# Optimization experiments

Measured on AMD Instinct MI355X. Metric: run time of the kernel, lower is better.

## Reference

```python
import jax, jax.numpy as jnp
import numpy as np

N, T, DF, H, NH, E = 512, 60, 6, 64, 2, 8192
NEG = -1e10

def _leaky(x):
    return jnp.where(x >= 0, x, 0.01 * x)

def _ln(x, g, b, eps=1e-5):
    m = x.mean(-1, keepdims=True)
    v = ((x - m) ** 2).mean(-1, keepdims=True)
    return (x - m) / jnp.sqrt(v + eps) * g + b

def _gru_layer(xs, wih, whh, bih, bhh):
    # xs: (N, T, H_in) -> (N, T, H); torch GRU gate math
    h0 = jnp.zeros((xs.shape[0], whh.shape[1]), xs.dtype)
    def step(h, xt):
        gi = xt @ wih.T + bih
        gh = h @ whh.T + bhh
        ir, iz, inn = jnp.split(gi, 3, -1)
        hr, hz, hn = jnp.split(gh, 3, -1)
        r = jax.nn.sigmoid(ir + hr)
        z = jax.nn.sigmoid(iz + hz)
        n = jnp.tanh(inn + r * hn)
        h = (1 - z) * n + z * h
        return h, h
    _, hs = jax.lax.scan(step, h0, jnp.swapaxes(xs, 0, 1))
    return jnp.swapaxes(hs, 0, 1)

def _forward(x, edge_index, fc_in_w, fc_in_b, gru_wih0, gru_whh0, gru_bih0, gru_bhh0, gru_wih1, gru_whh1, gru_bih1, gru_bhh1, dm_qw, dm_kw, dm_vw, dm_vb, ssa_qw, ssa_kw, ssa_vw, ssa_vb, ln1_g, ln1_b, ln2_g, ln2_b, mlp_w1, mlp_b1, mlp_w2, mlp_b2, mha_in_w, mha_in_b, mha_out_w, mha_out_b, gf_xs_w, gf_xt_w, gf_xt_b, gf_h_w, gf_h_b, lin_w, lin_b):
    h = x @ fc_in_w.T + fc_in_b                      # (N, T, H)
    # temporal encoder: 2-layer GRU + leaky relu
    g = _gru_layer(h, gru_wih0, gru_whh0, gru_bih0, gru_bhh0)
    g = _gru_layer(g, gru_wih1, gru_whh1, gru_bih1, gru_bhh1)
    ts = _leaky(g)
    res_ts = ts[:, -1, :]                            # (N, H)
    # spatial sparse transformer: time T acts as batch, attention over stocks N
    xs = jnp.swapaxes(h, 0, 1)                       # (T, N, H)
    hd = H // NH
    q = (xs @ dm_qw.T).reshape(T, N, NH, hd).transpose(0, 2, 1, 3)
    k = (xs @ dm_kw.T).reshape(T, N, NH, hd).transpose(0, 2, 1, 3)
    v = (xs @ dm_vw.T + dm_vb).reshape(T, N, NH, hd).transpose(0, 2, 1, 3)
    attn = jnp.einsum('thnd,thmd->thnm', q, k) * (H ** -0.5)  # scale uses full dim C, as in source
    dmask = attn >= attn.mean(-1, keepdims=True)     # dynamic per-row mean threshold
    attn_s = jax.nn.softmax(jnp.where(dmask, attn, NEG), axis=-1)
    dyn = jnp.einsum('thnm,thmd->thnd', attn_s, v).transpose(0, 2, 1, 3).reshape(T, N, H)
    # SSA: static graph mask from edge_index
    qs = xs @ ssa_qw.T
    ks2 = xs @ ssa_kw.T
    vs = xs @ ssa_vw.T + ssa_vb
    a2 = jnp.einsum('tnc,tmc->tnm', qs, ks2) * (H ** -0.5)
    adj = jnp.zeros((N, N), jnp.float32).at[edge_index[0], edge_index[1]].add(1.0)
    gmask = adj >= 1.0
    a2s = jax.nn.softmax(jnp.where(gmask[None, :, :], a2, NEG), axis=-1)
    stat = jnp.einsum('tnm,tmc->tnc', a2s, vs)
    residual = dyn + stat + xs
    o = _ln(residual, ln1_g, ln1_b)
    o = (o @ mlp_w1.T + mlp_b1) @ mlp_w2.T + mlp_b2  # two linears, no activation (as in source)
    o = _ln(o + residual, ln2_g, ln2_b)
    move = _leaky(o)                                 # (T, N, H)
    # spatial embedding aggregation: sinusoidal PE + 1-head MHA over time
    pos = jnp.arange(T, dtype=jnp.float32)[:, None]
    div = jnp.exp(jnp.arange(0, H, 2, dtype=jnp.float32) * (-np.log(10000.0) / H))
    pe = jnp.zeros((T, H), jnp.float32).at[:, 0::2].set(jnp.sin(pos * div)).at[:, 1::2].set(jnp.cos(pos * div))
    src = move + pe[:, None, :]
    mq, mk, mv = jnp.split(src @ mha_in_w.T + mha_in_b, 3, axis=-1)
    sc = jnp.einsum('tnh,snh->nts', mq, mk) * (H ** -0.5)
    mo = jnp.einsum('nts,snh->tnh', jax.nn.softmax(sc, -1), mv) @ mha_out_w.T + mha_out_b
    agg = mo[-1]                                     # (N, H)
    mu = agg.mean(-1, keepdims=True)
    var = ((agg - mu) ** 2).mean(-1, keepdims=True)
    agg = (agg - mu) / jnp.sqrt(var + 1e-5)          # param-free layer_norm
    # gated fusion
    zg = jax.nn.sigmoid(agg @ gf_xs_w.T + res_ts @ gf_xt_w.T + gf_xt_b)
    fused = _leaky((zg * agg + (1 - zg) * res_ts) @ gf_h_w.T + gf_h_b)
    out = (fused @ lin_w.T + lin_b)[:, 0]
    return out, attn_s

def setup_inputs() -> dict:
    key = jax.random.key(0)
    ks = jax.random.split(key, 40)
    def w(i, shape):
        return jax.random.normal(ks[i], shape, jnp.float32) * 0.05
    return {
        'x': jax.random.normal(ks[0], (N, T, DF), jnp.float32),
        'edge_index': jax.random.randint(ks[1], (2, E), 0, N),
        'fc_in_w': w(2, (H, DF)), 'fc_in_b': w(3, (H,)),
        'gru_wih0': w(4, (3 * H, H)), 'gru_whh0': w(5, (3 * H, H)), 'gru_bih0': w(6, (3 * H,)), 'gru_bhh0': w(7, (3 * H,)),
        'gru_wih1': w(8, (3 * H, H)), 'gru_whh1': w(9, (3 * H, H)), 'gru_bih1': w(10, (3 * H,)), 'gru_bhh1': w(11, (3 * H,)),
        'dm_qw': w(12, (H, H)), 'dm_kw': w(13, (H, H)), 'dm_vw': w(14, (H, H)), 'dm_vb': w(15, (H,)),
        'ssa_qw': w(16, (H, H)), 'ssa_kw': w(17, (H, H)), 'ssa_vw': w(18, (H, H)), 'ssa_vb': w(19, (H,)),
        'ln1_g': jnp.ones((H,), jnp.float32), 'ln1_b': jnp.zeros((H,), jnp.float32),
        'ln2_g': jnp.ones((H,), jnp.float32), 'ln2_b': jnp.zeros((H,), jnp.float32),
        'mlp_w1': w(20, (2 * H, H)), 'mlp_b1': w(21, (2 * H,)), 'mlp_w2': w(22, (H, 2 * H)), 'mlp_b2': w(23, (H,)),
        'mha_in_w': w(24, (3 * H, H)), 'mha_in_b': w(25, (3 * H,)), 'mha_out_w': w(26, (H, H)), 'mha_out_b': w(27, (H,)),
        'gf_xs_w': w(28, (H, H)), 'gf_xt_w': w(29, (H, H)), 'gf_xt_b': w(30, (H,)),
        'gf_h_w': w(31, (H, H)), 'gf_h_b': w(32, (H,)),
        'lin_w': w(33, (1, H)), 'lin_b': w(34, (1,)),
    }

def reference(x, edge_index, fc_in_w, fc_in_b, gru_wih0, gru_whh0, gru_bih0, gru_bhh0, gru_wih1, gru_whh1, gru_bih1, gru_bhh1, dm_qw, dm_kw, dm_vw, dm_vb, ssa_qw, ssa_kw, ssa_vw, ssa_vb, ln1_g, ln1_b, ln2_g, ln2_b, mlp_w1, mlp_b1, mlp_w2, mlp_b2, mha_in_w, mha_in_b, mha_out_w, mha_out_b, gf_xs_w, gf_xt_w, gf_xt_b, gf_h_w, gf_h_b, lin_w, lin_b):
    return _forward(x, edge_index, fc_in_w, fc_in_b, gru_wih0, gru_whh0, gru_bih0, gru_bhh0, gru_wih1, gru_whh1, gru_bih1, gru_bhh1, dm_qw, dm_kw, dm_vw, dm_vb, ssa_qw, ssa_kw, ssa_vw, ssa_vb, ln1_g, ln1_b, ln2_g, ln2_b, mlp_w1, mlp_b1, mlp_w2, mlp_b2, mha_in_w, mha_in_b, mha_out_w, mha_out_b, gf_xs_w, gf_xt_w, gf_xt_b, gf_h_w, gf_h_b, lin_w, lin_b)
```

## Files before the change

kernel.cpp:

```cpp
#include <hip/hip_runtime.h>
#include <hip/hip_bf16.h>

#define NN 512
#define TT 60
#define DFF 6
#define EE 8192
#define TN (TT*NN)
#define TCH 20
#define NCHK 3
#define SCALEV 0.125f
#define NEGV -1.0e10f

typedef __hip_bfloat16 bf16;
using bfrag8 = __attribute__((ext_vector_type(8))) short;
using facc4  = __attribute__((ext_vector_type(4))) float;

__device__ __forceinline__ float b2f(bf16 v){ return __bfloat162float(v); }
__device__ __forceinline__ bf16 f2b(float v){ return __float2bfloat16(v); }
__device__ __forceinline__ float lk(float x){ return x >= 0.f ? x : 0.01f*x; }
__device__ __forceinline__ float sgm(float x){ return 1.f/(1.f+__expf(-x)); }

__device__ __forceinline__ float ldf(const float* p, long i){ return p[i]; }
__device__ __forceinline__ float ldf(const bf16* p, long i){ return b2f(p[i]); }
__device__ __forceinline__ void stf(float* p, long i, float v){ p[i] = v; }
__device__ __forceinline__ void stf(bf16* p, long i, float v){ p[i] = f2b(v); }

__device__ __forceinline__ float4 ld4f(const float* p){ return *(const float4*)p; }
__device__ __forceinline__ float4 ld4f(const bf16* p){
  ushort4 u = *(const ushort4*)p;
  float4 f;
  f.x = b2f(*(const bf16*)&u.x);
  f.y = b2f(*(const bf16*)&u.y);
  f.z = b2f(*(const bf16*)&u.z);
  f.w = b2f(*(const bf16*)&u.w);
  return f;
}

__device__ __forceinline__ float wsum64(float v){
  #pragma unroll
  for (int off = 32; off; off >>= 1) v += __shfl_xor(v, off, 64);
  return v;
}
__device__ __forceinline__ float wmax64(float v){
  #pragma unroll
  for (int off = 32; off; off >>= 1) v = fmaxf(v, __shfl_xor(v, off, 64));
  return v;
}

__global__ __launch_bounds__(256) void k_pack(
  const float* __restrict__ qw, const float* __restrict__ kw,
  const float* __restrict__ qsw, const float* __restrict__ ksw,
  const float* __restrict__ vw, const float* __restrict__ vsw,
  const float* __restrict__ vb, const float* __restrict__ vsb,
  const int* __restrict__ ei, unsigned int* __restrict__ msk,
  float* __restrict__ Wall, float* __restrict__ bcV)
{
  __shared__ unsigned int lmsk[8192];
  int tid = threadIdx.x;
  if (blockIdx.x == 97) {
    for (int i = tid; i < 8192; i += 256) lmsk[i] = 0u;
    __syncthreads();
    for (int e = tid; e < EE; e += 256) {
      int u = ei[e], v = ei[EE + e];
      atomicOr(&lmsk[u*16 + (v >> 5)], 1u << (v & 31));
    }
    __syncthreads();
    for (int i = tid; i < 8192; i += 256) msk[i] = lmsk[i];
    return;
  }
  int idx = blockIdx.x*256 + tid;
  if (idx < 6*4096) {
    int which = idx >> 12, rem = idx & 4095;
    const float* s = (which==0)?qw:(which==1)?kw:(which==2)?qsw:(which==3)?ksw:(which==4)?vw:vsw;
    Wall[idx] = s[rem];
  } else if (idx < 6*4096 + 128) {
    int o = idx - 6*4096;
    bcV[o] = (o < 64) ? vb[o] : vsb[o-64];
  }
}

__global__ __launch_bounds__(256) void k_fcin(
  const float* __restrict__ x, const float* __restrict__ w, const float* __restrict__ b,
  float* __restrict__ xs, float* __restrict__ resid)
{
  long idx = (long)blockIdx.x*256 + threadIdx.x;
  int o = idx & 63;
  long r = idx >> 6;
  int t = (int)(r / NN), n = (int)(r % NN);
  const float* xr = x + ((long)n*TT + t)*DFF;
  const float* wr = w + o*DFF;
  float acc = 0.f;
  #pragma unroll
  for (int j = 0; j < DFF; ++j) acc = fmaf(xr[j], wr[j], acc);
  float h = __fadd_rn(acc, b[o]);
  xs[idx] = h;
  resid[idx] = h;
}

__global__ __launch_bounds__(256) void k_proj(
  const float* __restrict__ A, const float* __restrict__ Wall, const float* __restrict__ bcV,
  float* __restrict__ qkx, float* __restrict__ qkc, bf16* __restrict__ vvc)
{
  __shared__ float As[64][68];
  __shared__ float Bs[64][68];
  int rt = blockIdx.x, bcn = blockIdx.y;
  const float* B = Wall + bcn*4096;
  int tid = threadIdx.x;
  int tx = tid & 15, ty = tid >> 4;
  float acc[4][4] = {{0.f}};
  #pragma unroll
  for (int i = 0; i < 4; ++i) {
    int t = i*256 + tid;
    int m = t >> 4, kq = (t & 15)*4;
    float4 av = *(const float4*)&A[(long)(rt*64 + m)*64 + kq];
    As[kq+0][m] = av.x; As[kq+1][m] = av.y; As[kq+2][m] = av.z; As[kq+3][m] = av.w;
    float4 bv = *(const float4*)&B[(long)m*64 + kq];
    Bs[kq+0][m] = bv.x; Bs[kq+1][m] = bv.y; Bs[kq+2][m] = bv.z; Bs[kq+3][m] = bv.w;
  }
  __syncthreads();
  for (int kk = 0; kk < 64; ++kk) {
    float4 a4 = *(const float4*)&As[kk][ty*4];
    float4 b4 = *(const float4*)&Bs[kk][tx*4];
    acc[0][0] = fmaf(a4.x,b4.x,acc[0][0]); acc[0][1] = fmaf(a4.x,b4.y,acc[0][1]); acc[0][2] = fmaf(a4.x,b4.z,acc[0][2]); acc[0][3] = fmaf(a4.x,b4.w,acc[0][3]);
    acc[1][0] = fmaf(a4.y,b4.x,acc[1][0]); acc[1][1] = fmaf(a4.y,b4.y,acc[1][1]); acc[1][2] = fmaf(a4.y,b4.z,acc[1][2]); acc[1][3] = fmaf(a4.y,b4.w,acc[1][3]);
    acc[2][0] = fmaf(a4.z,b4.x,acc[2][0]); acc[2][1] = fmaf(a4.z,b4.y,acc[2][1]); acc[2][2] = fmaf(a4.z,b4.z,acc[2][2]); acc[2][3] = fmaf(a4.z,b4.w,acc[2][3]);
    acc[3][0] = fmaf(a4.w,b4.x,acc[3][0]); acc[3][1] = fmaf(a4.w,b4.y,acc[3][1]); acc[3][2] = fmaf(a4.w,b4.z,acc[3][2]); acc[3][3] = fmaf(a4.w,b4.w,acc[3][3]);
  }
  if (bcn < 4) {
    float* C = (bcn < 2) ? qkx : qkc;
    int cb = (bcn & 1)*64;
    #pragma unroll
    for (int i = 0; i < 4; ++i) {
      long ro = (long)(rt*64 + ty*4 + i)*128 + cb + tx*4;
      #pragma unroll
      for (int j = 0; j < 4; ++j) C[ro + j] = acc[i][j];
    }
  } else {
    int cb = (bcn - 4)*64;
    float bv[4];
    #pragma unroll
    for (int j = 0; j < 4; ++j) bv[j] = bcV[cb + tx*4 + j];
    #pragma unroll
    for (int i = 0; i < 4; ++i) {
      long ro = (long)(rt*64 + ty*4 + i)*128 + cb + tx*4;
      #pragma unroll
      for (int j = 0; j < 4; ++j) vvc[ro + j] = f2b(acc[i][j] + bv[j]);
    }
  }
}

template<typename TA, typename TC>
__global__ __launch_bounds__(256) void k_gemm(
  const TA* __restrict__ A, const float* __restrict__ B, const float* __restrict__ bias,
  TC* __restrict__ C, int KD, int NC, int gather)
{
  __shared__ float As[64][68];
  __shared__ float Bs[64][68];
  int rt = blockIdx.x, bcn = blockIdx.y;
  int tid = threadIdx.x;
  int tx = tid & 15, ty = tid >> 4;
  float acc[4][4] = {{0.f}};
  int nch = KD >> 6;
  for (int kc = 0; kc < nch; ++kc) {
    __syncthreads();
    #pragma unroll
    for (int i = 0; i < 4; ++i) {
      int t = i*256 + tid;
      int m = t >> 4, kq = (t & 15)*4;
      long aoff;
      int r = rt*64 + m;
      if (gather) { int n2 = r / TT, t2 = r - n2*TT; aoff = ((long)t2*NN + n2)*64 + kc*64 + kq; }
      else aoff = (long)r*KD + kc*64 + kq;
      float4 av = ld4f(A + aoff);
      As[kq+0][m] = av.x; As[kq+1][m] = av.y; As[kq+2][m] = av.z; As[kq+3][m] = av.w;
      int col = bcn*64 + m;
      float4 bv = *(const float4*)&B[(long)col*KD + kc*64 + kq];
      Bs[kq+0][m] = bv.x; Bs[kq+1][m] = bv.y; Bs[kq+2][m] = bv.z; Bs[kq+3][m] = bv.w;
    }
    __syncthreads();
    #pragma unroll 8
    for (int kk = 0; kk < 64; ++kk) {
      float4 a4 = *(const float4*)&As[kk][ty*4];
      float4 b4 = *(const float4*)&Bs[kk][tx*4];
      acc[0][0] += a4.x*b4.x; acc[0][1] += a4.x*b4.y; acc[0][2] += a4.x*b4.z; acc[0][3] += a4.x*b4.w;
      acc[1][0] += a4.y*b4.x; acc[1][1] += a4.y*b4.y; acc[1][2] += a4.y*b4.z; acc[1][3] += a4.y*b4.w;
      acc[2][0] += a4.z*b4.x; acc[2][1] += a4.z*b4.y; acc[2][2] += a4.z*b4.z; acc[2][3] += a4.z*b4.w;
      acc[3][0] += a4.w*b4.x; acc[3][1] += a4.w*b4.y; acc[3][2] += a4.w*b4.z; acc[3][3] += a4.w*b4.w;
    }
  }
  float bv[4];
  #pragma unroll
  for (int j = 0; j < 4; ++j) bv[j] = bias ? bias[bcn*64 + tx*4 + j] : 0.f;
  #pragma unroll
  for (int i = 0; i < 4; ++i) {
    long ro = (long)(rt*64 + ty*4 + i)*NC + bcn*64 + tx*4;
    #pragma unroll
    for (int j = 0; j < 4; ++j) stf(C, ro + j, acc[i][j] + bv[j]);
  }
}

__global__ __launch_bounds__(192) void k_gru(
  const float* __restrict__ gi, const float* __restrict__ whh, const float* __restrict__ bhh,
  bf16* __restrict__ g_out, float* __restrict__ res_out, int layer)
{
  int n = blockIdx.x;
  int tid = threadIdx.x;
  int g = tid >> 6, o = tid & 63;
  __shared__ __align__(16) float h_lds[64];
  __shared__ float ghs[3][64];
  float4 w4[16];
  #pragma unroll
  for (int k4 = 0; k4 < 16; ++k4)
    w4[k4] = *(const float4*)&whh[(long)(g*64+o)*64 + k4*4];
  float bh = bhh[g*64+o];
  float ir = 0.f, iz = 0.f, inn = 0.f;
  if (tid < 64) {
    h_lds[tid] = 0.f;
    const float* gp = gi + ((long)n*TT + 0)*192;
    ir = gp[o]; iz = gp[64+o]; inn = gp[128+o];
  }
  __syncthreads();
  const float4* h4 = (const float4*)h_lds;
  for (int t = 0; t < TT; ++t) {
    float p0 = 0.f, p1 = 0.f, p2 = 0.f, p3 = 0.f;
    #pragma unroll
    for (int k4 = 0; k4 < 16; ++k4) {
      float4 hv = h4[k4];
      p0 = fmaf(w4[k4].x, hv.x, p0);
      p1 = fmaf(w4[k4].y, hv.y, p1);
      p2 = fmaf(w4[k4].z, hv.z, p2);
      p3 = fmaf(w4[k4].w, hv.w, p3);
    }
    ghs[g][o] = bh + ((p0 + p1) + (p2 + p3));
    __syncthreads();
    if (tid < 64) {
      float r = sgm(ir + ghs[0][o]);
      float z = sgm(iz + ghs[1][o]);
      float nn2 = tanhf(inn + r*ghs[2][o]);
      float hn = (1.f - z)*nn2 + z*h_lds[o];
      h_lds[o] = hn;
      if (layer == 0) g_out[((long)t*NN + n)*64 + o] = f2b(hn);
      else if (t == TT-1) res_out[(long)n*64 + o] = lk(hn);
      if (t + 1 < TT) {
        const float* gp = gi + ((long)n*TT + t + 1)*192;
        ir = gp[o]; iz = gp[64+o]; inn = gp[128+o];
      }
    }
    __syncthreads();
  }
}

#define MULADD4(QV, KV) \
  v0 = __fadd_rn(v0, __fmul_rn((QV).x, (KV).x)); \
  v1 = __fadd_rn(v1, __fmul_rn((QV).y, (KV).y)); \
  v2 = __fadd_rn(v2, __fmul_rn((QV).z, (KV).z)); \
  v3 = __fadd_rn(v3, __fmul_rn((QV).w, (KV).w));

__global__ __launch_bounds__(256, 3) void k_attn(
  const float* __restrict__ qkx, const float* __restrict__ qkc,
  const bf16* __restrict__ vvc, const unsigned int* __restrict__ msk,
  float* __restrict__ attn_out, float* __restrict__ resid,
  float* __restrict__ resid2, int tc)
{
  __shared__ __align__(16) char smem[52288];
  int bid = blockIdx.x;
  int vid = (bid & 7)*240 + (bid >> 3);
  int lt = vid / 96;
  int rem = vid - lt*96;
  int yy = rem >> 5;
  int qt = rem & 31;
  int gt = tc*TCH + lt;
  int tid = threadIdx.x, tx = tid & 31, grp = tid >> 5;
  int qbase = grp*2;

  if (yy == 2) {
    float* kc  = (float*)smem;
    bf16*  vTh = (bf16*)smem;
    float* qtl = (float*)(smem + 34816);
    bf16*  P   = (bf16*)(smem + 34816);

    float4* q4 = (float4*)qtl;
    float4* k4 = (float4*)kc;

    {
      int m = tid >> 4, jc = tid & 15;
      q4[m*17 + jc] = *(const float4*)(qkc + ((long)(lt*NN + qt*16 + m))*128 + jc*4);
    }

    float S[2][16];
    for (int p = 0; p < 4; ++p) {
      __syncthreads();
      for (int i = tid; i < 2048; i += 256) {
        int m = i >> 4, jc = i & 15;
        k4[m*17 + (jc ^ ((m >> 2) & 3))] =
          *(const float4*)(qkc + ((long)(lt*NN + p*128 + m))*128 + 64 + jc*4);
      }
      __syncthreads();
      float acc00 = 0.f, acc01 = 0.f, acc02 = 0.f, acc03 = 0.f;
      float acc10 = 0.f, acc11 = 0.f, acc12 = 0.f, acc13 = 0.f;
      #pragma unroll 4
      for (int jc = 0; jc < 16; ++jc) {
        float4 q0 = q4[(qbase+0)*17 + jc];
        float4 q1 = q4[(qbase+1)*17 + jc];
        float4 kv;
        int m0 = tx;
        kv = k4[m0*17 + (jc ^ ((m0 >> 2) & 3))];
        acc00 += q0.x*kv.x + q0.y*kv.y + q0.z*kv.z + q0.w*kv.w;
        acc10 += q1.x*kv.x + q1.y*kv.y + q1.z*kv.z + q1.w*kv.w;
        int m1 = tx + 32;
        kv = k4[m1*17 + (jc ^ ((m1 >> 2) & 3))];
        acc01 += q0.x*kv.x + q0.y*kv.y + q0.z*kv.z + q0.w*kv.w;
        acc11 += q1.x*kv.x + q1.y*kv.y + q1.z*kv.z + q1.w*kv.w;
        int m2 = tx + 64;
        kv = k4[m2*17 + (jc ^ ((m2 >> 2) & 3))];
        acc02 += q0.x*kv.x + q0.y*kv.y + q0.z*kv.z + q0.w*kv.w;
        acc12 += q1.x*kv.x + q1.y*kv.y + q1.z*kv.z + q1.w*kv.w;
        int m3 = tx + 96;
        kv = k4[m3*17 + (jc ^ ((m3 >> 2) & 3))];
        acc03 += q0.x*kv.x + q0.y*kv.y + q0.z*kv.z + q0.w*kv.w;
        acc13 += q1.x*kv.x + q1.y*kv.y + q1.z*kv.z + q1.w*kv.w;
      }
      S[0][p*4+0] = acc00; S[0][p*4+1] = acc01; S[0][p*4+2] = acc02; S[0][p*4+3] = acc03;
      S[1][p*4+0] = acc10; S[1][p*4+1] = acc11; S[1][p*4+2] = acc12; S[1][p*4+3] = acc13;
    }
    __syncthreads();

    #pragma unroll
    for (int qi = 0; qi < 2; ++qi) {
      #pragma unroll
      for (int ig = 0; ig < 16; ++ig) S[qi][ig] *= SCALEV;
      float lm = -INFINITY;
      #pragma unroll
      for (int ig = 0; ig < 16; ++ig) {
        bool keep = ((msk[(qt*16 + qbase + qi)*16 + ig] >> tx) & 1u) != 0u;
        float v = keep ? S[qi][ig] : NEGV;
        S[qi][ig] = v;
        lm = fmaxf(lm, v);
      }
      #pragma unroll
      for (int mk = 1; mk < 32; mk <<= 1) lm = fmaxf(lm, __shfl_xor(lm, mk, 64));
      float se = 0.f;
      #pragma unroll
      for (int ig = 0; ig < 16; ++ig) {
        float ev = __expf(S[qi][ig] - lm);
        S[qi][ig] = ev;
        se += ev;
      }
      #pragma unroll
      for (int mk = 1; mk < 32; mk <<= 1) se += __shfl_xor(se, mk, 64);
      float inv = 1.f / se;
      bf16* prow = P + (qbase + qi)*520;
      #pragma unroll
      for (int ig = 0; ig < 16; ++ig)
        prow[tx + 32*ig] = f2b(S[qi][ig]*inv);
    }

    int w = tid >> 6, l = tid & 63;
    int arow = l & 15, kgrp = l >> 4;
    facc4 acc = {0.f, 0.f, 0.f, 0.f};
    for (int kh = 0; kh < 2; ++kh) {
      __syncthreads();
      for (int i = tid; i < 2048; i += 256) {
        int m2 = (i & 127) << 1;
        int cc = (i >> 7) << 2;
        const bf16* gp = vvc + ((long)(lt*NN + kh*256 + m2))*128 + 64 + cc;
        ushort4 a = *(const ushort4*)(gp);
        ushort4 b = *(const ushort4*)(gp + 128);
        *(unsigned*)(vTh + (cc+0)*264 + m2) = (unsigned)a.x | ((unsigned)b.x << 16);
        *(unsigned*)(vTh + (cc+1)*264 + m2) = (unsigned)a.y | ((unsigned)b.y << 16);
        *(unsigned*)(vTh + (cc+2)*264 + m2) = (unsigned)a.z | ((unsigned)b.z << 16);
        *(unsigned*)(vTh + (cc+3)*264 + m2) = (unsigned)a.w | ((unsigned)b.w << 16);
      }
      __syncthreads();
      const bf16* pa = P + arow*520 + kh*256 + kgrp*8;
      const bf16* pb = vTh + (w*16 + arow)*264 + kgrp*8;
      #pragma unroll
      for (int ks = 0; ks < 8; ++ks) {
        bfrag8 av = *(const bfrag8*)(pa + ks*32);
        bfrag8 bv = *(const bfrag8*)(pb + ks*32);
        acc = __builtin_amdgcn_mfma_f32_16x16x32_bf16(av, bv, acc, 0, 0, 0);
      }
    }
    long rb = ((long)gt*NN + qt*16)*64 + w*16 + arow;
    #pragma unroll
    for (int r = 0; r < 4; ++r) {
      int row = kgrp*4 + r;
      resid2[rb + (long)row*64] = acc[r];
    }
    return;
  }

  float* sc    = (float*)smem;
  bf16*  vT    = (bf16*)smem;
  float* kt    = (float*)(smem + 33280);
  bf16*  p_lds = (bf16*)(smem + 33280);
  float* red   = (float*)(smem + 49920);
  float* ulds  = (float*)(smem + 51712);
  float* means = (float*)(smem + 52224);

  int h = yy;
  int qce = h*32, kce = 64 + h*32;

  float4 q0r[8], q1r[8];
  {
    const float* qp = qkx + ((long)(lt*NN + qt*16 + qbase))*128 + qce;
    #pragma unroll
    for (int j = 0; j < 8; ++j) q0r[j] = *(const float4*)(qp + j*4);
    #pragma unroll
    for (int j = 0; j < 8; ++j) q1r[j] = *(const float4*)(qp + 128 + j*4);
  }

  float S[2][16];
  for (int p = 0; p < 4; ++p) {
    __syncthreads();
    for (int i = tid; i < 1024; i += 256) {
      int row = i >> 3, jj = (i & 7) << 2;
      *(float4*)(kt + row*36 + jj) =
        *(const float4*)(qkx + ((long)(lt*NN + p*128 + row))*128 + kce + jj);
    }
    __syncthreads();
    #pragma unroll
    for (int ii = 0; ii < 4; ++ii) {
      int m = tx + 32*ii;
      const float4* kr4 = (const float4*)(kt + m*36);
      float4 k0 = kr4[0], k1 = kr4[1], k2 = kr4[2], k3 = kr4[3];
      float4 k4 = kr4[4], k5 = kr4[5], k6 = kr4[6], k7 = kr4[7];
      {
        float v0 = 0.f, v1 = 0.f, v2 = 0.f, v3 = 0.f;
        MULADD4(q0r[0], k0); MULADD4(q0r[1], k1); MULADD4(q0r[2], k2); MULADD4(q0r[3], k3);
        MULADD4(q0r[4], k4); MULADD4(q0r[5], k5); MULADD4(q0r[6], k6); MULADD4(q0r[7], k7);
        float s = __fadd_rn(__fadd_rn(v0, v1), __fadd_rn(v2, v3));
        s = s * 0.125f;
        S[0][p*4+ii] = s;
        sc[(qbase+0)*520 + p*128 + m] = s;
      }
      {
        float v0 = 0.f, v1 = 0.f, v2 = 0.f, v3 = 0.f;
        MULADD4(q1r[0], k0); MULADD4(q1r[1], k1); MULADD4(q1r[2], k2); MULADD4(q1r[3], k3);
        MULADD4(q1r[4], k4); MULADD4(q1r[5], k5); MULADD4(q1r[6], k6); MULADD4(q1r[7], k7);
        float s = __fadd_rn(__fadd_rn(v0, v1), __fadd_rn(v2, v3));
        s = s * 0.125f;
        S[1][p*4+ii] = s;
        sc[(qbase+1)*520 + p*128 + m] = s;
      }
    }
  }
  __syncthreads();
  if (tid < 128) {
    int row = tid >> 3, b = (tid >> 1) & 3, hh = tid & 1;
    const float* a = sc + row*520 + b*128 + hh*4;
    float4 r4 = *(const float4*)a;
    #pragma unroll
    for (int i = 8; i < 128; i += 8) {
      float4 v = *(const float4*)(a + i);
      r4.x = __fadd_rn(r4.x, v.x); r4.y = __fadd_rn(r4.y, v.y);
      r4.z = __fadd_rn(r4.z, v.z); r4.w = __fadd_rn(r4.w, v.w);
    }
    ulds[row*8 + b*2 + hh] = __fadd_rn(__fadd_rn(r4.x, r4.y), __fadd_rn(r4.z, r4.w));
  }
  __syncthreads();
  if (tid < 16) {
    const float* ur = ulds + tid*8;
    float p0 = __fadd_rn(ur[0], ur[1]);
    float p1 = __fadd_rn(ur[2], ur[3]);
    float p2 = __fadd_rn(ur[4], ur[5]);
    float p3 = __fadd_rn(ur[6], ur[7]);
    means[tid] = __fadd_rn(__fadd_rn(p0, p1), __fadd_rn(p2, p3)) * (1.f/512.f);
  }
  __syncthreads();

  long obase = ((long)(gt*2 + h))*NN*NN;
  #pragma unroll
  for (int qi = 0; qi < 2; ++qi) {
    float mn = means[qbase + qi];
    unsigned kmask = 0; float lm = -INFINITY;
    #pragma unroll
    for (int ig = 0; ig < 16; ++ig) {
      if (S[qi][ig] >= mn) { kmask |= (1u << ig); lm = fmaxf(lm, S[qi][ig]); }
    }
    #pragma unroll
    for (int mk = 1; mk < 32; mk <<= 1) lm = fmaxf(lm, __shfl_xor(lm, mk, 64));
    float e[16]; float se = 0.f;
    #pragma unroll
    for (int ig = 0; ig < 16; ++ig) {
      e[ig] = ((kmask >> ig) & 1u) ? __expf(S[qi][ig] - lm) : 0.f;
      se += e[ig];
    }
    #pragma unroll
    for (int mk = 1; mk < 32; mk <<= 1) se += __shfl_xor(se, mk, 64);
    float inv = 1.f/se;
    float* rowp = attn_out + obase + (long)(qt*16 + qbase + qi)*NN;
    bf16* prow = p_lds + (qbase + qi)*520;
    #pragma unroll
    for (int ig = 0; ig < 16; ++ig) {
      float pr = e[ig]*inv;
      __builtin_nontemporal_store(pr, rowp + tx + 32*ig);
      prow[tx + 32*ig] = f2b(pr);
    }
  }

  for (int i = tid; i < 2048; i += 256) {
    int m2 = (i & 255) << 1;
    int cc = (i >> 8) << 2;
    const bf16* gp = vvc + ((long)(lt*NN + m2))*128 + qce + cc;
    ushort4 a = *(const ushort4*)(gp);
    ushort4 b = *(const ushort4*)(gp + 128);
    *(unsigned*)(vT + (cc+0)*520 + m2) = (unsigned)a.x | ((unsigned)b.x << 16);
    *(unsigned*)(vT + (cc+1)*520 + m2) = (unsigned)a.y | ((unsigned)b.y << 16);
    *(unsigned*)(vT + (cc+2)*520 + m2) = (unsigned)a.z | ((unsigned)b.z << 16);
    *(unsigned*)(vT + (cc+3)*520 + m2) = (unsigned)a.w | ((unsigned)b.w << 16);
  }
  __syncthreads();

  {
    int w = tid >> 6, l = tid & 63;
    int nh = w & 1, kh = w >> 1;
    int arow = l & 15, kgrp = l >> 4;
    facc4 acc = {0.f, 0.f, 0.f, 0.f};
    const bf16* pa = p_lds + arow*520 + kh*256 + kgrp*8;
    const bf16* pb = vT + (nh*16 + arow)*520 + kh*256 + kgrp*8;
    #pragma unroll
    for (int ks = 0; ks < 8; ++ks) {
      bfrag8 av = *(const bfrag8*)(pa + ks*32);
      bfrag8 bv = *(const bfrag8*)(pb + ks*32);
      acc = __builtin_amdgcn_mfma_f32_16x16x32_bf16(av, bv, acc, 0, 0, 0);
    }
    if (w >= 2) {
      #pragma unroll
      for (int r = 0; r < 4; ++r)
        red[nh*272 + (kgrp*4 + r)*17 + arow] = acc[r];
    }
    __syncthreads();
    if (w < 2) {
      long rb = ((long)gt*NN + qt*16)*64 + h*32 + nh*16 + arow;
      #pragma unroll
      for (int r = 0; r < 4; ++r) {
        int row = kgrp*4 + r;
        resid[rb + (long)row*64] += acc[r] + red[nh*272 + row*17 + arow];
      }
    }
  }
}

__global__ __launch_bounds__(256) void k_mlp1(
  const float* __restrict__ resid, const float* __restrict__ resid2,
  const float* __restrict__ g1, const float* __restrict__ b1,
  const float* __restrict__ B, const float* __restrict__ bias, float* __restrict__ C)
{
  __shared__ float As[64][68];
  __shared__ float Bs[64][68];
  int rt = blockIdx.x, bcn = blockIdx.y;
  int tid = threadIdx.x;
  int tx = tid & 15, ty = tid >> 4;
  int wave = tid >> 6, lane = tid & 63;
  for (int rr = wave; rr < 64; rr += 4) {
    long idx = ((long)rt*64 + rr)*64 + lane;
    float v = resid[idx] + resid2[idx];
    float m = wsum64(v)*(1.f/64.f);
    float d = v - m;
    float var = wsum64(d*d)*(1.f/64.f);
    As[lane][rr] = d*rsqrtf(var + 1e-5f)*g1[lane] + b1[lane];
  }
  #pragma unroll
  for (int i = 0; i < 4; ++i) {
    int t = i*256 + tid;
    int m = t >> 4, kq = (t & 15)*4;
    float4 bv = *(const float4*)&B[(long)(bcn*64 + m)*64 + kq];
    Bs[kq+0][m] = bv.x; Bs[kq+1][m] = bv.y; Bs[kq+2][m] = bv.z; Bs[kq+3][m] = bv.w;
  }
  __syncthreads();
  float acc[4][4] = {{0.f}};
  #pragma unroll 8
  for (int kk = 0; kk < 64; ++kk) {
    float4 a4 = *(const float4*)&As[kk][ty*4];
    float4 b4 = *(const float4*)&Bs[kk][tx*4];
    acc[0][0] += a4.x*b4.x; acc[0][1] += a4.x*b4.y; acc[0][2] += a4.x*b4.z; acc[0][3] += a4.x*b4.w;
    acc[1][0] += a4.y*b4.x; acc[1][1] += a4.y*b4.y; acc[1][2] += a4.y*b4.z; acc[1][3] += a4.y*b4.w;
    acc[2][0] += a4.z*b4.x; acc[2][1] += a4.z*b4.y; acc[2][2] += a4.z*b4.z; acc[2][3] += a4.z*b4.w;
    acc[3][0] += a4.w*b4.x; acc[3][1] += a4.w*b4.y; acc[3][2] += a4.w*b4.z; acc[3][3] += a4.w*b4.w;
  }
  #pragma unroll
  for (int i = 0; i < 4; ++i) {
    long ro = (long)(rt*64 + ty*4 + i)*128 + bcn*64 + tx*4;
    #pragma unroll
    for (int j = 0; j < 4; ++j) C[ro + j] = acc[i][j] + bias[bcn*64 + tx*4 + j];
  }
}

__global__ __launch_bounds__(256) void k_mha_in(
  const float* __restrict__ mlpo, const float* __restrict__ resid,
  const float* __restrict__ resid2,
  const float* __restrict__ g2, const float* __restrict__ b2,
  const float* __restrict__ B, const float* __restrict__ bias, bf16* __restrict__ C)
{
  __shared__ float As[64][68];
  __shared__ float Bs[64][68];
  int rt = blockIdx.x, bcn = blockIdx.y;
  int tid = threadIdx.x;
  int tx = tid & 15, ty = tid >> 4;
  int wave = tid >> 6, lane = tid & 63;
  for (int rr = wave; rr < 64; rr += 4) {
    long r = (long)rt*64 + rr;
    float rf = resid[r*64 + lane] + resid2[r*64 + lane];
    float v = mlpo[r*64 + lane] + rf;
    float m = wsum64(v)*(1.f/64.f);
    float d = v - m;
    float var = wsum64(d*d)*(1.f/64.f);
    float y = d*rsqrtf(var + 1e-5f)*g2[lane] + b2[lane];
    y = lk(y);
    float tf = (float)(r / NN);
    float dv = __expf(-(float)(lane & ~1) * 0.14391156831212787f);
    float pe = (lane & 1) ? cosf(tf*dv) : sinf(tf*dv);
    As[lane][rr] = y + pe;
  }
  #pragma unroll
  for (int i = 0; i < 4; ++i) {
    int t = i*256 + tid;
    int m = t >> 4, kq = (t & 15)*4;
    float4 bv = *(const float4*)&B[(long)(bcn*64 + m)*64 + kq];
    Bs[kq+0][m] = bv.x; Bs[kq+1][m] = bv.y; Bs[kq+2][m] = bv.z; Bs[kq+3][m] = bv.w;
  }
  __syncthreads();
  float acc[4][4] = {{0.f}};
  #pragma unroll 8
  for (int kk = 0; kk < 64; ++kk) {
    float4 a4 = *(const float4*)&As[kk][ty*4];
    float4 b4 = *(const float4*)&Bs[kk][tx*4];
    acc[0][0] += a4.x*b4.x; acc[0][1] += a4.x*b4.y; acc[0][2] += a4.x*b4.z; acc[0][3] += a4.x*b4.w;
    acc[1][0] += a4.y*b4.x; acc[1][1] += a4.y*b4.y; acc[1][2] += a4.y*b4.z; acc[1][3] += a4.y*b4.w;
    acc[2][0] += a4.z*b4.x; acc[2][1] += a4.z*b4.y; acc[2][2] += a4.z*b4.z; acc[2][3] += a4.z*b4.w;
    acc[3][0] += a4.w*b4.x; acc[3][1] += a4.w*b4.y; acc[3][2] += a4.w*b4.z; acc[3][3] += a4.w*b4.w;
  }
  #pragma unroll
  for (int i = 0; i < 4; ++i) {
    long ro = (long)(rt*64 + ty*4 + i)*192 + bcn*64 + tx*4;
    #pragma unroll
    for (int j = 0; j < 4; ++j) C[ro + j] = f2b(acc[i][j] + bias[bcn*64 + tx*4 + j]);
  }
}

__global__ __launch_bounds__(64) void k_head(
  const bf16* __restrict__ mqkv, const float* __restrict__ rts,
  const float* __restrict__ mow, const float* __restrict__ mob,
  const float* __restrict__ xsw, const float* __restrict__ xtw, const float* __restrict__ xtb,
  const float* __restrict__ hw, const float* __restrict__ hb,
  const float* __restrict__ linw, const float* __restrict__ linb,
  float* __restrict__ out)
{
  int n = blockIdx.x, o = threadIdx.x;
  __shared__ float ps[TT];
  __shared__ float buf[64], buf2[64];
  float mq = b2f(mqkv[((long)(TT-1)*NN + n)*192 + o]);
  for (int s = 0; s < TT; ++s) {
    float v = mq * b2f(mqkv[((long)s*NN + n)*192 + 64 + o]);
    v = wsum64(v);
    if (o == 0) ps[s] = v * SCALEV;
  }
  __syncthreads();
  float x = (o < TT) ? ps[o] : -INFINITY;
  float mx = wmax64(x);
  float e = (o < TT) ? __expf(x - mx) : 0.f;
  float se = wsum64(e);
  if (o < TT) ps[o] = e / se;
  __syncthreads();
  float acc = 0.f;
  for (int s = 0; s < TT; ++s) acc += ps[s]*b2f(mqkv[((long)s*NN + n)*192 + 128 + o]);
  buf[o] = acc;
  __syncthreads();
  float acc2 = mob[o];
  for (int k = 0; k < 64; ++k) acc2 += buf[k]*mow[o*64 + k];
  float m2 = wsum64(acc2)*(1.f/64.f);
  float d2 = acc2 - m2;
  float var2 = wsum64(d2*d2)*(1.f/64.f);
  float a = d2*rsqrtf(var2 + 1e-5f);
  float rt = rts[(long)n*64 + o];
  __syncthreads();
  buf[o] = a; buf2[o] = rt;
  __syncthreads();
  float pre = xtb[o];
  for (int k = 0; k < 64; ++k) pre += buf[k]*xsw[o*64 + k] + buf2[k]*xtw[o*64 + k];
  float zg = sgm(pre);
  float u = zg*a + (1.f - zg)*rt;
  __syncthreads();
  buf[o] = u;
  __syncthreads();
  float f = hb[o];
  for (int k = 0; k < 64; ++k) f += buf[k]*hw[o*64 + k];
  f = lk(f);
  float tot = wsum64(f * linw[o]);
  if (o == 0) out[n] = tot + linb[0];
}

extern "C" void kernel_launch(void* const* d_in, const int* in_sizes, int n_in,
                              void* d_out, int out_size, void* d_ws, size_t ws_size,
                              hipStream_t stream)
{
  const float* x    = (const float*)d_in[0];
  const int*   ei   = (const int*)  d_in[1];
  const float* fcw  = (const float*)d_in[2];
  const float* fcb  = (const float*)d_in[3];
  const float* wih0 = (const float*)d_in[4];
  const float* whh0 = (const float*)d_in[5];
  const float* bih0 = (const float*)d_in[6];
  const float* bhh0 = (const float*)d_in[7];
  const float* wih1 = (const float*)d_in[8];
  const float* whh1 = (const float*)d_in[9];
  const float* bih1 = (const float*)d_in[10];
  const float* bhh1 = (const float*)d_in[11];
  const float* dmqw = (const float*)d_in[12];
  const float* dmkw = (const float*)d_in[13];
  const float* dmvw = (const float*)d_in[14];
  const float* dmvb = (const float*)d_in[15];
  const float* ssqw = (const float*)d_in[16];
  const float* sskw = (const float*)d_in[17];
  const float* ssvw = (const float*)d_in[18];
  const float* ssvb = (const float*)d_in[19];
  const float* ln1g = (const float*)d_in[20];
  const float* ln1b = (const float*)d_in[21];
  const float* ln2g = (const float*)d_in[22];
  const float* ln2b = (const float*)d_in[23];
  const float* mw1  = (const float*)d_in[24];
  const float* mb1  = (const float*)d_in[25];
  const float* mw2  = (const float*)d_in[26];
  const float* mb2  = (const float*)d_in[27];
  const float* mhw  = (const float*)d_in[28];
  const float* mhb  = (const float*)d_in[29];
  const float* mow  = (const float*)d_in[30];
  const float* mob  = (const float*)d_in[31];
  const float* gxsw = (const float*)d_in[32];
  const float* gxtw = (const float*)d_in[33];
  const float* gxtb = (const float*)d_in[34];
  const float* ghw  = (const float*)d_in[35];
  const float* ghb  = (const float*)d_in[36];
  const float* linw = (const float*)d_in[37];
  const float* linb = (const float*)d_in[38];

  char* base = (char*)d_ws;
  float*  xs    = (float*)(base);
  char*   Rb    = base + 7864320;
  float*  qkc   = (float*)Rb;
  bf16*   vvc   = (bf16*)(Rb + 5242880);
  float*  qkx   = (float*)(Rb + 7864320);
  float*  mlph  = (float*)Rb;
  bf16*   mqkv  = (bf16*)Rb;
  bf16*   g0    = (bf16*)(base + 23592960);
  float*  resid = (float*)(base + 27525120);
  float*  resid2= (float*)(base + 35389440);
  float*  rts   = (float*)(base + 43253760);
  unsigned int* msk = (unsigned int*)(base + 43384832);
  float*  Wall  = (float*)(base + 43417600);
  float*  bcV   = (float*)(base + 43515904);
  float*  mlpo  = xs;
  float*  outb  = (float*)d_out;
  float*  attn  = outb + 512;
  float*  gi    = (float*)((char*)d_out + 2048);

  k_pack<<<dim3(98), 256, 0, stream>>>(dmqw, dmkw, ssqw, sskw, dmvw, ssvw, dmvb, ssvb, ei, msk, Wall, bcV);
  k_fcin<<<dim3(TN*64/256), 256, 0, stream>>>(x, fcw, fcb, xs, resid);
  k_gemm<float,float><<<dim3(480, 3), 256, 0, stream>>>(xs, wih0, bih0, gi, 64, 192, 1);
  k_gru<<<dim3(NN), 192, 0, stream>>>(gi, whh0, bhh0, g0, nullptr, 0);
  k_gemm<bf16,float><<<dim3(480, 3), 256, 0, stream>>>(g0, wih1, bih1, gi, 64, 192, 1);
  k_gru<<<dim3(NN), 192, 0, stream>>>(gi, whh1, bhh1, nullptr, rts, 1);
  for (int tc = 0; tc < NCHK; ++tc) {
    const float* xsc = xs + (size_t)tc*TCH*NN*64;
    k_proj<<<dim3(TCH*NN/64, 6), 256, 0, stream>>>(xsc, Wall, bcV, qkx, qkc, vvc);
    k_attn<<<dim3(1920), 256, 0, stream>>>(qkx, qkc, vvc, msk, attn, resid, resid2, tc);
  }
  k_mlp1<<<dim3(480, 2), 256, 0, stream>>>(resid, resid2, ln1g, ln1b, mw1, mb1, mlph);
  k_gemm<float,float><<<dim3(480, 1), 256, 0, stream>>>(mlph, mw2, mb2, mlpo, 128, 64, 0);
  k_mha_in<<<dim3(480, 3), 256, 0, stream>>>(mlpo, resid, resid2, ln2g, ln2b, mhw, mhb, mqkv);
  k_head<<<dim3(NN), 64, 0, stream>>>(mqkv, rts, mow, mob, gxsw, gxtw, gxtb, ghw, ghb, linw, linb, outb);
}
```

Baseline: 735.2 us.

## Shrink attention LDS footprint to raise occupancy to four blocks per CU

Cuts shared memory per block from about 51KB to 36KB and raises the launch bound to 4 blocks per CU. To fit, K and V tiles are staged in smaller chunks, and the per-row score mean is now computed with wavefront shuffles instead of being written to LDS and reduced there. The added syncs and chunked loops cost some latency, and the tighter register budget may cause spills, in exchange for more resident waves to hide memory latency.

```diff
diff --git a/kernel.cpp b/kernel.cpp
--- a/kernel.cpp
+++ b/kernel.cpp
@@ -256,13 +256,13 @@
   v2 = __fadd_rn(v2, __fmul_rn((QV).z, (KV).z)); \
   v3 = __fadd_rn(v3, __fmul_rn((QV).w, (KV).w));
 
-__global__ __launch_bounds__(256, 3) void k_attn(
+__global__ __launch_bounds__(256, 4) void k_attn(
   const float* __restrict__ qkx, const float* __restrict__ qkc,
   const bf16* __restrict__ vvc, const unsigned int* __restrict__ msk,
   float* __restrict__ attn_out, float* __restrict__ resid,
   float* __restrict__ resid2, int tc)
 {
-  __shared__ __align__(16) char smem[52288];
+  __shared__ __align__(16) char smem[36864];
   int bid = blockIdx.x;
   int vid = (bid & 7)*240 + (bid >> 3);
   int lt = vid / 96;
@@ -275,9 +275,9 @@
 
   if (yy == 2) {
     float* kc  = (float*)smem;
-    bf16*  vTh = (bf16*)smem;
-    float* qtl = (float*)(smem + 34816);
-    bf16*  P   = (bf16*)(smem + 34816);
+    float* qtl = (float*)(smem + 17408);
+    bf16*  P   = (bf16*)smem;
+    bf16*  vTh = (bf16*)(smem + 16640);
 
     float4* q4 = (float4*)qtl;
     float4* k4 = (float4*)kc;
@@ -288,16 +288,17 @@
     }
 
     float S[2][16];
-    for (int p = 0; p < 4; ++p) {
+    #pragma unroll
+    for (int p2 = 0; p2 < 8; ++p2) {
       __syncthreads();
-      for (int i = tid; i < 2048; i += 256) {
+      for (int i = tid; i < 1024; i += 256) {
         int m = i >> 4, jc = i & 15;
         k4[m*17 + (jc ^ ((m >> 2) & 3))] =
-          *(const float4*)(qkc + ((long)(lt*NN + p*128 + m))*128 + 64 + jc*4);
+          *(const float4*)(qkc + ((long)(lt*NN + p2*64 + m))*128 + 64 + jc*4);
       }
       __syncthreads();
-      float acc00 = 0.f, acc01 = 0.f, acc02 = 0.f, acc03 = 0.f;
-      float acc10 = 0.f, acc11 = 0.f, acc12 = 0.f, acc13 = 0.f;
+      float acc00 = 0.f, acc01 = 0.f;
+      float acc10 = 0.f, acc11 = 0.f;
       #pragma unroll 4
       for (int jc = 0; jc < 16; ++jc) {
         float4 q0 = q4[(qbase+0)*17 + jc];
@@ -311,17 +312,9 @@
         kv = k4[m1*17 + (jc ^ ((m1 >> 2) & 3))];
         acc01 += q0.x*kv.x + q0.y*kv.y + q0.z*kv.z + q0.w*kv.w;
         acc11 += q1.x*kv.x + q1.y*kv.y + q1.z*kv.z + q1.w*kv.w;
-        int m2 = tx + 64;
-        kv = k4[m2*17 + (jc ^ ((m2 >> 2) & 3))];
-        acc02 += q0.x*kv.x + q0.y*kv.y + q0.z*kv.z + q0.w*kv.w;
-        acc12 += q1.x*kv.x + q1.y*kv.y + q1.z*kv.z + q1.w*kv.w;
-        int m3 = tx + 96;
-        kv = k4[m3*17 + (jc ^ ((m3 >> 2) & 3))];
-        acc03 += q0.x*kv.x + q0.y*kv.y + q0.z*kv.z + q0.w*kv.w;
-        acc13 += q1.x*kv.x + q1.y*kv.y + q1.z*kv.z + q1.w*kv.w;
-      }
-      S[0][p*4+0] = acc00; S[0][p*4+1] = acc01; S[0][p*4+2] = acc02; S[0][p*4+3] = acc03;
-      S[1][p*4+0] = acc10; S[1][p*4+1] = acc11; S[1][p*4+2] = acc12; S[1][p*4+3] = acc13;
+      }
+      S[0][p2*2+0] = acc00; S[0][p2*2+1] = acc01;
+      S[1][p2*2+0] = acc10; S[1][p2*2+1] = acc11;
     }
     __syncthreads();
 
@@ -358,24 +351,24 @@
     int w = tid >> 6, l = tid & 63;
     int arow = l & 15, kgrp = l >> 4;
     facc4 acc = {0.f, 0.f, 0.f, 0.f};
-    for (int kh = 0; kh < 2; ++kh) {
+    for (int kq = 0; kq < 4; ++kq) {
       __syncthreads();
-      for (int i = tid; i < 2048; i += 256) {
-        int m2 = (i & 127) << 1;
-        int cc = (i >> 7) << 2;
-        const bf16* gp = vvc + ((long)(lt*NN + kh*256 + m2))*128 + 64 + cc;
+      for (int i = tid; i < 1024; i += 256) {
+        int m2 = (i & 63) << 1;
+        int cc = (i >> 6) << 2;
+        const bf16* gp = vvc + ((long)(lt*NN + kq*128 + m2))*128 + 64 + cc;
         ushort4 a = *(const ushort4*)(gp);
         ushort4 b = *(const ushort4*)(gp + 128);
-        *(unsigned*)(vTh + (cc+0)*264 + m2) = (unsigned)a.x | ((unsigned)b.x << 16);
-        *(unsigned*)(vTh + (cc+1)*264 + m2) = (unsigned)a.y | ((unsigned)b.y << 16);
-        *(unsigned*)(vTh + (cc+2)*264 + m2) = (unsigned)a.z | ((unsigned)b.z << 16);
-        *(unsigned*)(vTh + (cc+3)*264 + m2) = (unsigned)a.w | ((unsigned)b.w << 16);
+        *(unsigned*)(vTh + (cc+0)*136 + m2) = (unsigned)a.x | ((unsigned)b.x << 16);
+        *(unsigned*)(vTh + (cc+1)*136 + m2) = (unsigned)a.y | ((unsigned)b.y << 16);
+        *(unsigned*)(vTh + (cc+2)*136 + m2) = (unsigned)a.z | ((unsigned)b.z << 16);
+        *(unsigned*)(vTh + (cc+3)*136 + m2) = (unsigned)a.w | ((unsigned)b.w << 16);
       }
       __syncthreads();
-      const bf16* pa = P + arow*520 + kh*256 + kgrp*8;
-      const bf16* pb = vTh + (w*16 + arow)*264 + kgrp*8;
-      #pragma unroll
-      for (int ks = 0; ks < 8; ++ks) {
+      const bf16* pa = P + arow*520 + kq*128 + kgrp*8;
+      const bf16* pb = vTh + (w*16 + arow)*136 + kgrp*8;
+      #pragma unroll
+      for (int ks = 0; ks < 4; ++ks) {
         bfrag8 av = *(const bfrag8*)(pa + ks*32);
         bfrag8 bv = *(const bfrag8*)(pb + ks*32);
         acc = __builtin_amdgcn_mfma_f32_16x16x32_bf16(av, bv, acc, 0, 0, 0);
@@ -390,13 +383,10 @@
     return;
   }
 
-  float* sc    = (float*)smem;
-  bf16*  vT    = (bf16*)smem;
-  float* kt    = (float*)(smem + 33280);
-  bf16*  p_lds = (bf16*)(smem + 33280);
-  float* red   = (float*)(smem + 49920);
-  float* ulds  = (float*)(smem + 51712);
-  float* means = (float*)(smem + 52224);
+  float* kt    = (float*)smem;
+  bf16*  p_lds = (bf16*)smem;
+  bf16*  vT2   = (bf16*)(smem + 16640);
+  float* red   = (float*)(smem + 33536);
 
   int h = yy;
   int qce = h*32, kce = 64 + h*32;
@@ -411,16 +401,17 @@
   }
 
   float S[2][16];
-  for (int p = 0; p < 4; ++p) {
-    __syncthreads();
-    for (int i = tid; i < 1024; i += 256) {
+  #pragma unroll
+  for (int P2 = 0; P2 < 2; ++P2) {
+    __syncthreads();
+    for (int i = tid; i < 2048; i += 256) {
       int row = i >> 3, jj = (i & 7) << 2;
       *(float4*)(kt + row*36 + jj) =
-        *(const float4*)(qkx + ((long)(lt*NN + p*128 + row))*128 + kce + jj);
-    }
-    __syncthreads();
-    #pragma unroll
-    for (int ii = 0; ii < 4; ++ii) {
+        *(const float4*)(qkx + ((long)(lt*NN + P2*256 + row))*128 + kce + jj);
+    }
+    __syncthreads();
+    #pragma unroll
+    for (int ii = 0; ii < 8; ++ii) {
       int m = tx + 32*ii;
       const float4* kr4 = (const float4*)(kt + m*36);
       float4 k0 = kr4[0], k1 = kr4[1], k2 = kr4[2], k3 = kr4[3];
@@ -430,49 +421,57 @@
         MULADD4(q0r[0], k0); MULADD4(q0r[1], k1); MULADD4(q0r[2], k2); MULADD4(q0r[3], k3);
         MULADD4(q0r[4], k4); MULADD4(q0r[5], k5); MULADD4(q0r[6], k6); MULADD4(q0r[7], k7);
         float s = __fadd_rn(__fadd_rn(v0, v1), __fadd_rn(v2, v3));
-        s = s * 0.125f;
-        S[0][p*4+ii] = s;
-        sc[(qbase+0)*520 + p*128 + m] = s;
+        S[0][P2*8+ii] = s * 0.125f;
       }
       {
         float v0 = 0.f, v1 = 0.f, v2 = 0.f, v3 = 0.f;
         MULADD4(q1r[0], k0); MULADD4(q1r[1], k1); MULADD4(q1r[2], k2); MULADD4(q1r[3], k3);
         MULADD4(q1r[4], k4); MULADD4(q1r[5], k5); MULADD4(q1r[6], k6); MULADD4(q1r[7], k7);
         float s = __fadd_rn(__fadd_rn(v0, v1), __fadd_rn(v2, v3));
-        s = s * 0.125f;
-        S[1][p*4+ii] = s;
-        sc[(qbase+1)*520 + p*128 + m] = s;
-      }
-    }
-  }
-  __syncthreads();
-  if (tid < 128) {
-    int row = tid >> 3, b = (tid >> 1) & 3, hh = tid & 1;
-    const float* a = sc + row*520 + b*128 + hh*4;
-    float4 r4 = *(const float4*)a;
-    #pragma unroll
-    for (int i = 8; i < 128; i += 8) {
-      float4 v = *(const float4*)(a + i);
-      r4.x = __fadd_rn(r4.x, v.x); r4.y = __fadd_rn(r4.y, v.y);
-      r4.z = __fadd_rn(r4.z, v.z); r4.w = __fadd_rn(r4.w, v.w);
-    }
-    ulds[row*8 + b*2 + hh] = __fadd_rn(__fadd_rn(r4.x, r4.y), __fadd_rn(r4.z, r4.w));
-  }
-  __syncthreads();
-  if (tid < 16) {
-    const float* ur = ulds + tid*8;
-    float p0 = __fadd_rn(ur[0], ur[1]);
-    float p1 = __fadd_rn(ur[2], ur[3]);
-    float p2 = __fadd_rn(ur[4], ur[5]);
-    float p3 = __fadd_rn(ur[6], ur[7]);
-    means[tid] = __fadd_rn(__fadd_rn(p0, p1), __fadd_rn(p2, p3)) * (1.f/512.f);
-  }
-  __syncthreads();
+        S[1][P2*8+ii] = s * 0.125f;
+      }
+    }
+  }
+  __syncthreads();
+
+  float mn0, mn1;
+  {
+    float pr0[4], pr1[4];
+    #pragma unroll
+    for (int b = 0; b < 4; ++b) {
+      float a0, a1;
+      #pragma unroll
+      for (int k = 0; k < 16; ++k) {
+        int src = (tid & 32) + (tid & 7) + 8*(k & 3);
+        float v0 = __shfl(S[0][b*4 + (k >> 2)], src, 64);
+        float v1 = __shfl(S[1][b*4 + (k >> 2)], src, 64);
+        if (k == 0) { a0 = v0; a1 = v1; }
+        else { a0 = __fadd_rn(a0, v0); a1 = __fadd_rn(a1, v1); }
+      }
+      int sb = tid & 32;
+      float g0 = __shfl(a0, sb+0, 64), g1 = __shfl(a0, sb+1, 64);
+      float g2 = __shfl(a0, sb+2, 64), g3 = __shfl(a0, sb+3, 64);
+      float g4 = __shfl(a0, sb+4, 64), g5 = __shfl(a0, sb+5, 64);
+      float g6 = __shfl(a0, sb+6, 64), g7 = __shfl(a0, sb+7, 64);
+      float u0 = __fadd_rn(__fadd_rn(g0, g1), __fadd_rn(g2, g3));
+      float u1 = __fadd_rn(__fadd_rn(g4, g5), __fadd_rn(g6, g7));
+      pr0[b] = __fadd_rn(u0, u1);
+      float t0 = __shfl(a1, sb+0, 64), t1 = __shfl(a1, sb+1, 64);
+      float t2 = __shfl(a1, sb+2, 64), t3 = __shfl(a1, sb+3, 64);
+      float t4 = __shfl(a1, sb+4, 64), t5 = __shfl(a1, sb+5, 64);
+      float t6 = __shfl(a1, sb+6, 64), t7 = __shfl(a1, sb+7, 64);
+      float w0 = __fadd_rn(__fadd_rn(t0, t1), __fadd_rn(t2, t3));
+      float w1 = __fadd_rn(__fadd_rn(t4, t5), __fadd_rn(t6, t7));
+      pr1[b] = __fadd_rn(w0, w1);
+    }
+    mn0 = __fadd_rn(__fadd_rn(pr0[0], pr0[1]), __fadd_rn(pr0[2], pr0[3])) * (1.f/512.f);
+    mn1 = __fadd_rn(__fadd_rn(pr1[0], pr1[1]), __fadd_rn(pr1[2], pr1[3])) * (1.f/512.f);
+  }
 
   long obase = ((long)(gt*2 + h))*NN*NN;
   #pragma unroll
   for (int qi = 0; qi < 2; ++qi) {
-    float mn = means[qbase + qi];
+    float mn = qi ? mn1 : mn0;
     unsigned kmask = 0; float lm = -INFINITY;
     #pragma unroll
     for (int ig = 0; ig < 16; ++ig) {
@@ -499,31 +498,33 @@
     }
   }
 
-  for (int i = tid; i < 2048; i += 256) {
-    int m2 = (i & 255) << 1;
-    int cc = (i >> 8) << 2;
-    const bf16* gp = vvc + ((long)(lt*NN + m2))*128 + qce + cc;
-    ushort4 a = *(const ushort4*)(gp);
-    ushort4 b = *(const ushort4*)(gp + 128);
-    *(unsigned*)(vT + (cc+0)*520 + m2) = (unsigned)a.x | ((unsigned)b.x << 16);
-    *(unsigned*)(vT + (cc+1)*520 + m2) = (unsigned)a.y | ((unsigned)b.y << 16);
-    *(unsigned*)(vT + (cc+2)*520 + m2) = (unsigned)a.z | ((unsigned)b.z << 16);
-    *(unsigned*)(vT + (cc+3)*520 + m2) = (unsigned)a.w | ((unsigned)b.w << 16);
-  }
-  __syncthreads();
-
   {
     int w = tid >> 6, l = tid & 63;
-    int nh = w & 1, kh = w >> 1;
+    int nh = w & 1, kg = w >> 1;
     int arow = l & 15, kgrp = l >> 4;
     facc4 acc = {0.f, 0.f, 0.f, 0.f};
-    const bf16* pa = p_lds + arow*520 + kh*256 + kgrp*8;
-    const bf16* pb = vT + (nh*16 + arow)*520 + kh*256 + kgrp*8;
-    #pragma unroll
-    for (int ks = 0; ks < 8; ++ks) {
-      bfrag8 av = *(const bfrag8*)(pa + ks*32);
-      bfrag8 bv = *(const bfrag8*)(pb + ks*32);
-      acc = __builtin_amdgcn_mfma_f32_16x16x32_bf16(av, bv, acc, 0, 0, 0);
+    for (int kh = 0; kh < 2; ++kh) {
+      __syncthreads();
+      for (int i = tid; i < 1024; i += 256) {
+        int m2 = (i & 127) << 1;
+        int cc = (i >> 7) << 2;
+        const bf16* gp = vvc + ((long)(lt*NN + kh*256 + m2))*128 + qce + cc;
+        ushort4 a = *(const ushort4*)(gp);
+        ushort4 b = *(const ushort4*)(gp + 128);
+        *(unsigned*)(vT2 + (cc+0)*264 + m2) = (unsigned)a.x | ((unsigned)b.x << 16);
+        *(unsigned*)(vT2 + (cc+1)*264 + m2) = (unsigned)a.y | ((unsigned)b.y << 16);
+        *(unsigned*)(vT2 + (cc+2)*264 + m2) = (unsigned)a.z | ((unsigned)b.z << 16);
+        *(unsigned*)(vT2 + (cc+3)*264 + m2) = (unsigned)a.w | ((unsigned)b.w << 16);
+      }
+      __syncthreads();
+      const bf16* pa = p_lds + arow*520 + kh*256 + kg*128 + kgrp*8;
+      const bf16* pb = vT2 + (nh*16 + arow)*264 + kg*128 + kgrp*8;
+      #pragma unroll
+      for (int ks = 0; ks < 4; ++ks) {
+        bfrag8 av = *(const bfrag8*)(pa + ks*32);
+        bfrag8 bv = *(const bfrag8*)(pb + ks*32);
+        acc = __builtin_amdgcn_mfma_f32_16x16x32_bf16(av, bv, acc, 0, 0, 0);
+      }
     }
     if (w >= 2) {
       #pragma unroll
```

Measured after the change: 2.327 ms. +216.6%, slower.
